# Performance work log

Measured on AMD Instinct MI355X. Metric: run time of the kernel, lower is better.

Reference implementation:

```python
import jax, jax.numpy as jnp
import numpy as np

N_USERS = 100000
N_ITEMS = 100000
N_BICLIQUES = 50000
NNZ = 2000000
D = 64


def setup_inputs() -> dict:
    key = jax.random.key(0)
    k1, k2, k3, k4, k5, k6 = jax.random.split(key, 6)
    return {
        "user_emb": jax.random.normal(k1, (N_USERS, D), dtype=jnp.float32),
        "item_emb": jax.random.normal(k2, (N_ITEMS, D), dtype=jnp.float32),
        "hv_rows": jax.random.randint(k3, (NNZ,), 0, N_BICLIQUES, dtype=jnp.int32),
        "hv_cols": jax.random.randint(k4, (NNZ,), 0, N_ITEMS, dtype=jnp.int32),
        "hv_vals": jnp.ones((NNZ,), dtype=jnp.float32),
        "hu_rows": jax.random.randint(k5, (NNZ,), 0, N_USERS, dtype=jnp.int32),
        "hu_cols": jax.random.randint(k6, (NNZ,), 0, N_BICLIQUES, dtype=jnp.int32),
        "hu_vals": jnp.ones((NNZ,), dtype=jnp.float32),
        "n_bicliques": N_BICLIQUES,
        "n_users": N_USERS,
    }


def _spmm_mean(rows, cols, vals, dense, num_segments):
    # out[r] = (sum_{e: rows[e]==r} vals[e] * dense[cols[e]]) / max(degree[r], treat 0 as 1)
    # degree[r] = sum of vals on row r (matches torch.sparse.sum(dim=1)).
    num = jax.ops.segment_sum(vals[:, None] * dense[cols], rows, num_segments=num_segments)
    deg = jax.ops.segment_sum(vals, rows, num_segments=num_segments)
    deg = jnp.where(deg == 0, 1.0, deg)[:, None]
    return num / deg


def reference(user_emb, item_emb, hv_rows, hv_cols, hv_vals, hu_rows, hu_cols, hu_vals, n_bicliques, n_users):
    # Hop 1: biclique features = row-mean of item embeddings via H_v [n_bicliques, n_items]
    biclique_features = _spmm_mean(hv_rows, hv_cols, hv_vals, item_emb, n_bicliques)
    # Hop 2: user local view = row-mean of biclique features via H_u [n_users, n_bicliques]
    user_local_view = _spmm_mean(hu_rows, hu_cols, hu_vals, biclique_features, n_users)
    return user_local_view
```

## Files before the change

### kernel.cpp

```cpp
#include <hip/hip_runtime.h>
#include <hip/hip_fp16.h>


#define DIM 64
#define CAP 2944
#define CHUNK 8192
#define P1B 512
#define EPT (CHUNK / P1B)
#define NBIN 782
#define SH1 6
#define SH2 7
#define KR 6

__global__ __launch_bounds__(P1B) void pass1_bin_kernel(
    const int* __restrict__ rows1, const int* __restrict__ cols1,
    const float* __restrict__ vals1, int nnz1, int nc1, int ncb,
    const int* __restrict__ rows2, const int* __restrict__ cols2,
    const float* __restrict__ vals2, int nnz2,
    int* __restrict__ bincnt1, int2* __restrict__ st1,
    int* __restrict__ bincnt2, int2* __restrict__ st2,
    const float4* __restrict__ cvt_in, int2* __restrict__ cvt_out, int n4) {
    __shared__ int hist[NBIN];
    __shared__ int cur[NBIN];
    if ((int)blockIdx.x >= ncb) {
        int i0 = (blockIdx.x - ncb) * (P1B * 4) + threadIdx.x;
        #pragma unroll
        for (int k = 0; k < 4; ++k) {
            int i = i0 + k * P1B;
            if (i < n4) {
                float4 x = cvt_in[i];
                __half2 h0 = __float22half2_rn(make_float2(x.x, x.y));
                __half2 h1 = __float22half2_rn(make_float2(x.z, x.w));
                int2 pk;
                pk.x = *(int*)&h0;
                pk.y = *(int*)&h1;
                cvt_out[i] = pk;
            }
        }
        return;
    }
    const int* rows; const int* cols; const float* vals;
    int nnz, shift, chunk_id;
    int* bincnt; int2* st;
    if ((int)blockIdx.x < nc1) {
        rows = rows1; cols = cols1; vals = vals1; nnz = nnz1;
        shift = SH1; chunk_id = blockIdx.x; bincnt = bincnt1; st = st1;
    } else {
        rows = rows2; cols = cols2; vals = vals2; nnz = nnz2;
        shift = SH2; chunk_id = blockIdx.x - nc1; bincnt = bincnt2; st = st2;
    }
    int t = threadIdx.x;
    for (int i = t; i < NBIN; i += P1B) hist[i] = 0;
    __syncthreads();
    int begin = chunk_id * CHUNK;

    int r[EPT]; int c[EPT]; float v[EPT];
    #pragma unroll
    for (int k = 0; k < EPT; ++k) {
        int idx = begin + k * P1B + t;
        bool ok = idx < nnz;
        r[k] = ok ? rows[idx] : -1;
        c[k] = ok ? cols[idx] : 0;
        v[k] = ok ? vals[idx] : 0.0f;
        if (ok) atomicAdd(&hist[r[k] >> shift], 1);
    }
    __syncthreads();
    for (int i = t; i < NBIN; i += P1B) {
        int h = hist[i];
        if (h > 0) cur[i] = i * CAP + atomicAdd(&bincnt[i], h);
    }
    __syncthreads();
    #pragma unroll
    for (int k = 0; k < EPT; ++k) {
        if (r[k] >= 0) {
            int b = r[k] >> shift;
            int pos = atomicAdd(&cur[b], 1);
            int key = ((r[k] - (b << shift)) << 17) | c[k];
            st[pos] = make_int2(key, __float_as_int(v[k]));
        }
    }
}

template <int RPB, bool DST_HALF>
__global__ __launch_bounds__(512, 8) void sort_gather_kernel(
    const int2* __restrict__ st, const int* __restrict__ bincnt,
    const __half* __restrict__ src,
    void* __restrict__ dstv,
    int n_rows) {
    __shared__ int2 edges[CAP];
    __shared__ int excl[RPB];
    __shared__ int cur[RPB];
    __shared__ int wsum[2];
    const int b = blockIdx.x;
    const int t = threadIdx.x;
    const int row0 = b * RPB;
    int cnt_b = min(bincnt[b], CAP);
    const int2* bst = st + (size_t)b * CAP;

    if (t < RPB) cur[t] = 0;
    __syncthreads();
    int2 reg[KR];
    #pragma unroll
    for (int k = 0; k < KR; ++k) {
        int i = t + k * P1B;
        bool ok = i < cnt_b;
        reg[k] = ok ? bst[i] : make_int2(-1, 0);
        if (ok) atomicAdd(&cur[reg[k].x >> 17], 1);
    }
    __syncthreads();
    if (t < RPB) {
        int cc = cur[t];
        int x = cc;
        #pragma unroll
        for (int off = 1; off < 64; off <<= 1) {
            int n = __shfl_up(x, off);
            if ((t & 63) >= off) x += n;
        }
        excl[t] = x - cc;
        if (RPB > 64 && (t & 63) == 63) wsum[t >> 6] = x;
    }
    __syncthreads();
    if (t < RPB) {
        int e = excl[t];
        if (RPB > 64 && t >= 64) e += wsum[0];
        excl[t] = e;
        cur[t]  = e;
    }
    __syncthreads();
    #pragma unroll
    for (int k = 0; k < KR; ++k) {
        int key = reg[k].x;
        if (key >= 0) {
            int pos = atomicAdd(&cur[key >> 17], 1);
            edges[pos] = make_int2(key & 0x1FFFF, reg[k].y);
        }
    }
    __syncthreads();

    const int wave = t >> 6;
    const int lane = t & 63;
    const int sub = lane >> 4;
    const int ld  = lane & 15;
    const __half* srcl = src + ld * 4;
    for (int rl = wave; rl < RPB; rl += 8) {
        int row = row0 + rl;
        if (row >= n_rows) break;
        int start = excl[rl];
        int end   = cur[rl];
        float ax = 0.f, ay = 0.f, az = 0.f, aw = 0.f, vsum = 0.f;
        for (int i = start + sub; i < end; i += 16) {
            int lim = end - 1;
            int j1 = min(i + 4,  lim);
            int j2 = min(i + 8,  lim);
            int j3 = min(i + 12, lim);
            int2 e0 = edges[i];
            int2 e1 = edges[j1];
            int2 e2 = edges[j2];
            int2 e3 = edges[j3];
            float v0 = __int_as_float(e0.y);
            float v1 = (i + 4  < end) ? __int_as_float(e1.y) : 0.f;
            float v2 = (i + 8  < end) ? __int_as_float(e2.y) : 0.f;
            float v3 = (i + 12 < end) ? __int_as_float(e3.y) : 0.f;
            int2 r0 = *(const int2*)(srcl + (e0.x << 6));
            int2 r1 = *(const int2*)(srcl + (e1.x << 6));
            int2 r2 = *(const int2*)(srcl + (e2.x << 6));
            int2 r3 = *(const int2*)(srcl + (e3.x << 6));
            float2 a0 = __half22float2(*(__half2*)&r0.x);
            float2 b0 = __half22float2(*(__half2*)&r0.y);
            float2 a1 = __half22float2(*(__half2*)&r1.x);
            float2 b1 = __half22float2(*(__half2*)&r1.y);
            float2 a2 = __half22float2(*(__half2*)&r2.x);
            float2 b2 = __half22float2(*(__half2*)&r2.y);
            float2 a3 = __half22float2(*(__half2*)&r3.x);
            float2 b3 = __half22float2(*(__half2*)&r3.y);
            ax += v0 * a0.x + v1 * a1.x + v2 * a2.x + v3 * a3.x;
            ay += v0 * a0.y + v1 * a1.y + v2 * a2.y + v3 * a3.y;
            az += v0 * b0.x + v1 * b1.x + v2 * b2.x + v3 * b3.x;
            aw += v0 * b0.y + v1 * b1.y + v2 * b2.y + v3 * b3.y;
            vsum += (v0 + v1) + (v2 + v3);
        }
        #pragma unroll
        for (int off = 16; off <= 32; off <<= 1) {
            ax += __shfl_xor(ax, off);
            ay += __shfl_xor(ay, off);
            az += __shfl_xor(az, off);
            aw += __shfl_xor(aw, off);
            vsum += __shfl_xor(vsum, off);
        }
        float d = (vsum == 0.0f) ? 1.0f : vsum;
        if (sub == 0) {
            float inv = 1.0f / d;
            if (DST_HALF) {
                __half* dst = (__half*)dstv;
                __half2 o0 = __float22half2_rn(make_float2(ax * inv, ay * inv));
                __half2 o1 = __float22half2_rn(make_float2(az * inv, aw * inv));
                int2 pk;
                pk.x = *(int*)&o0;
                pk.y = *(int*)&o1;
                *(int2*)(dst + row * DIM + ld * 4) = pk;
            } else {
                float* dst = (float*)dstv;
                float4 o = make_float4(ax * inv, ay * inv, az * inv, aw * inv);
                *(float4*)(dst + row * DIM + ld * 4) = o;
            }
        }
    }
}

extern "C" void kernel_launch(void* const* d_in, const int* in_sizes, int n_in,
                              void* d_out, int out_size, void* d_ws, size_t ws_size,
                              hipStream_t stream) {
    const float* item_emb = (const float*)d_in[1];
    const int*   hv_rows  = (const int*)d_in[2];
    const int*   hv_cols  = (const int*)d_in[3];
    const float* hv_vals  = (const float*)d_in[4];
    const int*   hu_rows  = (const int*)d_in[5];
    const int*   hu_cols  = (const int*)d_in[6];
    const float* hu_vals  = (const float*)d_in[7];

    const int nnz1 = in_sizes[2];
    const int nnz2 = in_sizes[5];
    const int n_items = in_sizes[1] / DIM;
    const int n_b  = 50000;
    const int n_u  = out_size / DIM;

    float* out = (float*)d_out;

    char* p = (char*)d_ws;
    __half* item_h  = (__half*)p; p += (size_t)n_items * DIM * sizeof(__half);
    __half* bf_h    = (__half*)p; p += (size_t)n_b * DIM * sizeof(__half);
    int*   bincnt1 = (int*)p;   p += NBIN * sizeof(int);
    int*   bincnt2 = (int*)p;   p += NBIN * sizeof(int);
    int2*  st1     = (int2*)p;  p += (size_t)NBIN * CAP * sizeof(int2);
    int2*  st2     = (int2*)p;  p += (size_t)NBIN * CAP * sizeof(int2);

    hipMemsetAsync(bincnt1, 0, 2 * NBIN * sizeof(int), stream);

    int n4 = n_items * DIM / 4;
    int nc1 = (nnz1 + CHUNK - 1) / CHUNK;
    int nc2 = (nnz2 + CHUNK - 1) / CHUNK;
    int ncb = nc1 + nc2;
    int ncv = (n4 + P1B * 4 - 1) / (P1B * 4);

    pass1_bin_kernel<<<ncb + ncv, P1B, 0, stream>>>(
        hv_rows, hv_cols, hv_vals, nnz1, nc1, ncb,
        hu_rows, hu_cols, hu_vals, nnz2,
        bincnt1, st1, bincnt2, st2,
        (const float4*)item_emb, (int2*)item_h, n4);

    sort_gather_kernel<64, true><<<NBIN, 512, 0, stream>>>(
        st1, bincnt1, item_h, bf_h, n_b);
    sort_gather_kernel<128, false><<<NBIN, 512, 0, stream>>>(
        st2, bincnt2, bf_h, out, n_u);
}
```

Baseline: 252.3 us.

## Replace global atomic bin scatter with per-chunk local sort and offset tables

Pass 1 now sorts each chunk by bin in shared memory and writes it contiguously, together with a per-chunk offset table, instead of using global atomics to scatter edges into fixed-capacity bins. The gather kernels then prefix-sum per-chunk segment lengths and copy the matching segments from every chunk into shared memory before the row sort. This removes the memset and global atomic contention and makes pass-1 writes coalesced. In exchange, each gather block reads many small scattered segments (489 chunks of about 5 edges each) and adds extra scans and a shared staging copy. CHUNK is also halved.

```diff
diff --git a/kernel.cpp b/kernel.cpp
--- a/kernel.cpp
+++ b/kernel.cpp
@@ -4,26 +4,31 @@
 
 #define DIM 64
 #define CAP 2944
-#define CHUNK 8192
+#define CHUNK 4096
 #define P1B 512
 #define EPT (CHUNK / P1B)
 #define NBIN 782
 #define SH1 6
 #define SH2 7
-#define KR 6
-
-__global__ __launch_bounds__(P1B) void pass1_bin_kernel(
+#define PITCH (NBIN + 1)
+
+__global__ __launch_bounds__(P1B) void pass1_kernel(
     const int* __restrict__ rows1, const int* __restrict__ cols1,
     const float* __restrict__ vals1, int nnz1, int nc1, int ncb,
     const int* __restrict__ rows2, const int* __restrict__ cols2,
     const float* __restrict__ vals2, int nnz2,
-    int* __restrict__ bincnt1, int2* __restrict__ st1,
-    int* __restrict__ bincnt2, int2* __restrict__ st2,
+    int2* __restrict__ st1, int* __restrict__ ofs1,
+    int2* __restrict__ st2, int* __restrict__ ofs2,
     const float4* __restrict__ cvt_in, int2* __restrict__ cvt_out, int n4) {
+    __shared__ int2 sorted[CHUNK];
     __shared__ int hist[NBIN];
+    __shared__ int excl[NBIN];
     __shared__ int cur[NBIN];
+    __shared__ int wtot[9];
+    const int t = threadIdx.x;
+
     if ((int)blockIdx.x >= ncb) {
-        int i0 = (blockIdx.x - ncb) * (P1B * 4) + threadIdx.x;
+        int i0 = (blockIdx.x - ncb) * (P1B * 4) + t;
         #pragma unroll
         for (int k = 0; k < 4; ++k) {
             int i = i0 + k * P1B;
@@ -41,15 +46,14 @@
     }
     const int* rows; const int* cols; const float* vals;
     int nnz, shift, chunk_id;
-    int* bincnt; int2* st;
+    int2* st; int* ofs;
     if ((int)blockIdx.x < nc1) {
         rows = rows1; cols = cols1; vals = vals1; nnz = nnz1;
-        shift = SH1; chunk_id = blockIdx.x; bincnt = bincnt1; st = st1;
+        shift = SH1; chunk_id = blockIdx.x; st = st1; ofs = ofs1;
     } else {
         rows = rows2; cols = cols2; vals = vals2; nnz = nnz2;
-        shift = SH2; chunk_id = blockIdx.x - nc1; bincnt = bincnt2; st = st2;
-    }
-    int t = threadIdx.x;
+        shift = SH2; chunk_id = blockIdx.x - nc1; st = st2; ofs = ofs2;
+    }
     for (int i = t; i < NBIN; i += P1B) hist[i] = 0;
     __syncthreads();
     int begin = chunk_id * CHUNK;
@@ -65,75 +69,135 @@
         if (ok) atomicAdd(&hist[r[k] >> shift], 1);
     }
     __syncthreads();
-    for (int i = t; i < NBIN; i += P1B) {
-        int h = hist[i];
-        if (h > 0) cur[i] = i * CAP + atomicAdd(&bincnt[i], h);
-    }
+    int b0 = 2 * t;
+    int h0 = 0, pv = 0;
+    if (b0 < NBIN) {
+        h0 = hist[b0];
+        pv = h0 + ((b0 + 1 < NBIN) ? hist[b0 + 1] : 0);
+    }
+    int x = pv;
+    #pragma unroll
+    for (int o = 1; o < 64; o <<= 1) {
+        int n = __shfl_up(x, o);
+        if ((t & 63) >= o) x += n;
+    }
+    if ((t & 63) == 63) wtot[t >> 6] = x;
+    __syncthreads();
+    if (t == 0) {
+        int acc = 0;
+        #pragma unroll
+        for (int w = 0; w < 8; ++w) { int tmp = wtot[w]; wtot[w] = acc; acc += tmp; }
+        wtot[8] = acc;
+    }
+    __syncthreads();
+    int ex = x - pv + wtot[t >> 6];
+    if (b0 < NBIN) {
+        excl[b0] = ex; cur[b0] = ex;
+        if (b0 + 1 < NBIN) { excl[b0 + 1] = ex + h0; cur[b0 + 1] = ex + h0; }
+    }
+    const int chunk_len = wtot[8];
     __syncthreads();
     #pragma unroll
     for (int k = 0; k < EPT; ++k) {
         if (r[k] >= 0) {
-            int b = r[k] >> shift;
-            int pos = atomicAdd(&cur[b], 1);
-            int key = ((r[k] - (b << shift)) << 17) | c[k];
-            st[pos] = make_int2(key, __float_as_int(v[k]));
-        }
-    }
+            int bb = r[k] >> shift;
+            int pos = atomicAdd(&cur[bb], 1);
+            int key = ((r[k] - (bb << shift)) << 17) | c[k];
+            sorted[pos] = make_int2(key, __float_as_int(v[k]));
+        }
+    }
+    __syncthreads();
+    size_t cbase = (size_t)chunk_id * CHUNK;
+    for (int i = t; i < chunk_len; i += P1B) st[cbase + i] = sorted[i];
+    int* orow = ofs + (size_t)chunk_id * PITCH;
+    for (int i = t; i <= NBIN; i += P1B)
+        orow[i] = (i < NBIN) ? excl[i] : chunk_len;
 }
 
 template <int RPB, bool DST_HALF>
-__global__ __launch_bounds__(512, 8) void sort_gather_kernel(
-    const int2* __restrict__ st, const int* __restrict__ bincnt,
-    const __half* __restrict__ src,
-    void* __restrict__ dstv,
-    int n_rows) {
+__global__ __launch_bounds__(P1B) void sort_gather_kernel(
+    const int2* __restrict__ st, const int* __restrict__ ofs, int nc,
+    const __half* __restrict__ src, void* __restrict__ dstv, int n_rows) {
+    __shared__ int2 concat[CAP];
     __shared__ int2 edges[CAP];
+    __shared__ int dstA[P1B + 1];
+    __shared__ int sofs[P1B];
     __shared__ int excl[RPB];
     __shared__ int cur[RPB];
-    __shared__ int wsum[2];
+    __shared__ int wtot[9];
     const int b = blockIdx.x;
     const int t = threadIdx.x;
     const int row0 = b * RPB;
-    int cnt_b = min(bincnt[b], CAP);
-    const int2* bst = st + (size_t)b * CAP;
-
+
+    int so = 0, len = 0;
+    if (t < nc) {
+        const int* rowp = ofs + (size_t)t * PITCH + b;
+        so  = rowp[0];
+        len = rowp[1] - rowp[0];
+    }
     if (t < RPB) cur[t] = 0;
-    __syncthreads();
-    int2 reg[KR];
+    int x = len;
     #pragma unroll
-    for (int k = 0; k < KR; ++k) {
-        int i = t + k * P1B;
-        bool ok = i < cnt_b;
-        reg[k] = ok ? bst[i] : make_int2(-1, 0);
-        if (ok) atomicAdd(&cur[reg[k].x >> 17], 1);
+    for (int o = 1; o < 64; o <<= 1) {
+        int n = __shfl_up(x, o);
+        if ((t & 63) >= o) x += n;
+    }
+    if ((t & 63) == 63) wtot[t >> 6] = x;
+    __syncthreads();
+    if (t == 0) {
+        int acc = 0;
+        #pragma unroll
+        for (int w = 0; w < 8; ++w) { int tmp = wtot[w]; wtot[w] = acc; acc += tmp; }
+        wtot[8] = acc;
+    }
+    __syncthreads();
+    dstA[t] = x - len + wtot[t >> 6];
+    sofs[t] = so;
+    if (t == 0) dstA[P1B] = wtot[8];
+    const int cnt_b = min(wtot[8], CAP);
+    __syncthreads();
+
+    {
+        int g  = t >> 3;
+        int lg = t & 7;
+        for (int cs = g; cs < nc; cs += 64) {
+            int d0 = dstA[cs];
+            int L  = dstA[cs + 1] - d0;
+            const int2* sp = st + (size_t)cs * CHUNK + sofs[cs];
+            for (int i = lg; i < L; i += 8) {
+                int p = d0 + i;
+                if (p < CAP) {
+                    int2 ed = sp[i];
+                    concat[p] = ed;
+                    atomicAdd(&cur[ed.x >> 17], 1);
+                }
+            }
+        }
     }
     __syncthreads();
     if (t < RPB) {
         int cc = cur[t];
-        int x = cc;
-        #pragma unroll
-        for (int off = 1; off < 64; off <<= 1) {
-            int n = __shfl_up(x, off);
-            if ((t & 63) >= off) x += n;
-        }
-        excl[t] = x - cc;
-        if (RPB > 64 && (t & 63) == 63) wsum[t >> 6] = x;
+        int x2 = cc;
+        #pragma unroll
+        for (int o = 1; o < 64; o <<= 1) {
+            int n = __shfl_up(x2, o);
+            if ((t & 63) >= o) x2 += n;
+        }
+        excl[t] = x2 - cc;
+        if (RPB > 64 && (t & 63) == 63) wtot[t >> 6] = x2;
     }
     __syncthreads();
     if (t < RPB) {
         int e = excl[t];
-        if (RPB > 64 && t >= 64) e += wsum[0];
+        if (RPB > 64 && t >= 64) e += wtot[0];
         excl[t] = e;
         cur[t]  = e;
     }
     __syncthreads();
-    #pragma unroll
-    for (int k = 0; k < KR; ++k) {
-        int key = reg[k].x;
-        if (key >= 0) {
-            int pos = atomicAdd(&cur[key >> 17], 1);
-            edges[pos] = make_int2(key & 0x1FFFF, reg[k].y);
-        }
+    for (int i = t; i < cnt_b; i += P1B) {
+        int2 ed = concat[i];
+        int pos = atomicAdd(&cur[ed.x >> 17], 1);
+        edges[pos] = make_int2(ed.x & 0x1FFFF, ed.y);
     }
     __syncthreads();
 
@@ -226,30 +290,29 @@
 
     float* out = (float*)d_out;
 
-    char* p = (char*)d_ws;
-    __half* item_h  = (__half*)p; p += (size_t)n_items * DIM * sizeof(__half);
-    __half* bf_h    = (__half*)p; p += (size_t)n_b * DIM * sizeof(__half);
-    int*   bincnt1 = (int*)p;   p += NBIN * sizeof(int);
-    int*   bincnt2 = (int*)p;   p += NBIN * sizeof(int);
-    int2*  st1     = (int2*)p;  p += (size_t)NBIN * CAP * sizeof(int2);
-    int2*  st2     = (int2*)p;  p += (size_t)NBIN * CAP * sizeof(int2);
-
-    hipMemsetAsync(bincnt1, 0, 2 * NBIN * sizeof(int), stream);
-
-    int n4 = n_items * DIM / 4;
     int nc1 = (nnz1 + CHUNK - 1) / CHUNK;
     int nc2 = (nnz2 + CHUNK - 1) / CHUNK;
+
+    char* p = (char*)d_ws;
+    __half* item_h = (__half*)p; p += (size_t)n_items * DIM * sizeof(__half);
+    __half* bf_h   = (__half*)p; p += (size_t)n_b * DIM * sizeof(__half);
+    int2*  st1     = (int2*)p;   p += (size_t)nc1 * CHUNK * sizeof(int2);
+    int2*  st2     = (int2*)p;   p += (size_t)nc2 * CHUNK * sizeof(int2);
+    int*   ofs1    = (int*)p;    p += (size_t)nc1 * PITCH * sizeof(int);
+    int*   ofs2    = (int*)p;    p += (size_t)nc2 * PITCH * sizeof(int);
+
+    int n4 = n_items * DIM / 4;
     int ncb = nc1 + nc2;
     int ncv = (n4 + P1B * 4 - 1) / (P1B * 4);
 
-    pass1_bin_kernel<<<ncb + ncv, P1B, 0, stream>>>(
+    pass1_kernel<<<ncb + ncv, P1B, 0, stream>>>(
         hv_rows, hv_cols, hv_vals, nnz1, nc1, ncb,
         hu_rows, hu_cols, hu_vals, nnz2,
-        bincnt1, st1, bincnt2, st2,
+        st1, ofs1, st2, ofs2,
         (const float4*)item_emb, (int2*)item_h, n4);
 
-    sort_gather_kernel<64, true><<<NBIN, 512, 0, stream>>>(
-        st1, bincnt1, item_h, bf_h, n_b);
-    sort_gather_kernel<128, false><<<NBIN, 512, 0, stream>>>(
-        st2, bincnt2, bf_h, out, n_u);
+    sort_gather_kernel<64, true><<<NBIN, P1B, 0, stream>>>(
+        st1, ofs1, nc1, item_h, bf_h, n_b);
+    sort_gather_kernel<128, false><<<NBIN, P1B, 0, stream>>>(
+        st2, ofs2, nc2, bf_h, out, n_u);
 }
```

Result: slower. 259.6 us (+2.9%).
